# Performance work log

Hardware: AMD Instinct MI355X
Metric: run time of the kernel (lower is better)

Reference implementation:

```python
import jax, jax.numpy as jnp
import numpy as np
from jax import lax


def setup_inputs() -> dict:
    key = jax.random.key(0)
    ks = jax.random.split(key, 8)
    b, l, d_model = 2, 1024, 768
    expand, d_state, d_conv = 2, 16, 4
    d_inner = d_model * expand            # 1536
    dt_rank = -(-d_model // 16)           # ceil(768/16) = 48
    x = jax.random.normal(ks[0], (b, l, d_model), jnp.float32)
    W_in = jax.random.normal(ks[1], (d_model, 2 * d_inner), jnp.float32) * 0.02
    conv_w = jax.random.normal(ks[2], (d_inner, 1, d_conv), jnp.float32) * 0.1
    conv_b = jnp.zeros((d_inner,), jnp.float32)
    W_x = jax.random.normal(ks[3], (d_inner, dt_rank + 2 * d_state), jnp.float32) * 0.02
    W_dt = jax.random.normal(ks[4], (dt_rank, d_inner), jnp.float32) * 0.02
    b_dt = jax.random.normal(ks[5], (d_inner,), jnp.float32) * 0.02
    # A_log = log(1..d_state) broadcast over d_inner, as in the module init
    A_log = jnp.broadcast_to(jnp.log(jnp.arange(1, d_state + 1, dtype=jnp.float32)), (d_inner, d_state)).copy()
    D = jnp.ones((d_inner,), jnp.float32)
    W_out = jax.random.normal(ks[6], (d_inner, d_model), jnp.float32) * 0.02
    return {"x": x, "W_in": W_in, "conv_w": conv_w, "conv_b": conv_b, "W_x": W_x,
            "W_dt": W_dt, "b_dt": b_dt, "A_log": A_log, "D": D, "W_out": W_out}


def _silu(v):
    return v * jax.nn.sigmoid(v)


def reference(x, W_in, conv_w, conv_b, W_x, W_dt, b_dt, A_log, D, W_out):
    b, l, d_model = x.shape
    d_inner, _, d_conv = conv_w.shape
    dt_rank = W_dt.shape[0]
    n = A_log.shape[1]

    # in_proj and split into x / res paths
    x_and_res = x @ W_in                              # (b, l, 2*d_inner)
    xi, res = jnp.split(x_and_res, 2, axis=-1)

    # depthwise causal conv1d (torch pads d_conv-1 both sides then slices [:l])
    xc = jnp.transpose(xi, (0, 2, 1))                 # (b, d_inner, l)
    xc = lax.conv_general_dilated(
        xc, conv_w, window_strides=(1,), padding=[(d_conv - 1, 0)],
        dimension_numbers=("NCH", "OIH", "NCH"), feature_group_count=d_inner)
    xc = xc + conv_b[None, :, None]
    u = _silu(jnp.transpose(xc, (0, 2, 1)))           # (b, l, d_inner)

    # SSM parameters (input-dependent)
    A = -jnp.exp(A_log.astype(jnp.float32))           # (d_inner, n)
    x_dbl = u @ W_x                                   # (b, l, dt_rank + 2n)
    delta = x_dbl[..., :dt_rank]
    B = x_dbl[..., dt_rank:dt_rank + n]               # (b, l, n)
    C = x_dbl[..., dt_rank + n:]                      # (b, l, n)
    delta = jax.nn.softplus(delta @ W_dt + b_dt)      # (b, l, d_inner)

    # discretize
    deltaA = jnp.exp(delta[..., None] * A)            # (b, l, d_inner, n)
    deltaB_u = delta[..., None] * B[:, :, None, :] * u[..., None]  # (b, l, d_inner, n)

    # parallel associative scan over l: h_t = deltaA_t * h_{t-1} + deltaB_u_t
    def combine(c1, c2):
        a1, b1 = c1
        a2, b2 = c2
        return (a1 * a2, a2 * b1 + b2)

    _, hs = lax.associative_scan(combine, (deltaA, deltaB_u), axis=1)  # (b, l, d_inner, n)

    y = jnp.einsum("bldn,bln->bld", hs, C) + u * D    # (b, l, d_inner)
    y = y * _silu(res)
    out = y @ W_out                                   # (b, l, d_model)
    return out
```

## Files before the change

kernel.cpp:

```cpp
#include <hip/hip_runtime.h>
#include <math.h>

#define DI 1536
#define DM 768
#define NSTATE 16
#define DTRANK 48
#define LSEQ 1024
#define NBATCH 2
#define MROWS (NBATCH*LSEQ)
#define NXR 3072
#define NCHUNK 128
#define CLEN 8
#define SCB 128
#define DMP 16

typedef __attribute__((ext_vector_type(4))) float f32x4;
typedef __attribute__((ext_vector_type(8))) short s16x8;
typedef __attribute__((ext_vector_type(4))) unsigned int u32x4;

__device__ __forceinline__ unsigned short f2bf(float f) {
  unsigned int x = __builtin_bit_cast(unsigned int, f);
  return (unsigned short)((x + 0x7fffu + ((x >> 16) & 1u)) >> 16);
}

__device__ __forceinline__ void gload_lds16(const void* g, void* l) {
  __builtin_amdgcn_global_load_lds(
      (const __attribute__((address_space(1))) void*)g,
      (__attribute__((address_space(3))) void*)l, 16, 0, 0);
}

__global__ __launch_bounds__(256) void prep_kernel(
    const float* __restrict__ x, const float* __restrict__ W_in,
    const float* __restrict__ W_out, const float* __restrict__ W_x,
    const float* __restrict__ A_log,
    unsigned short* __restrict__ x_bf, unsigned short* __restrict__ WinT,
    unsigned short* __restrict__ WoutT, unsigned short* __restrict__ WxT,
    float* __restrict__ negA)
{
  __shared__ float t[32][33];
  const int bid = blockIdx.x;
  const int tid = threadIdx.x;
  if (bid < 768) {
    long i = ((long)bid * 256 + tid) * 8;
    f32x4 v0 = *(const f32x4*)&x[i];
    f32x4 v1 = *(const f32x4*)&x[i + 4];
    unsigned short o[8];
    #pragma unroll
    for (int j = 0; j < 4; ++j) { o[j] = f2bf(v0[j]); o[4 + j] = f2bf(v1[j]); }
    *(u32x4*)&x_bf[i] = *(u32x4*)o;
    return;
  }
  int tx = tid & 31, ty = tid >> 5;
  if (bid >= 4368) {
    int rtile = (bid - 4368) * 32;
    #pragma unroll
    for (int i = 0; i < 4; ++i) {
      int r = ty + i * 8;
      if (tx < 16) t[r][tx] = A_log[(long)(rtile + r) * NSTATE + tx];
    }
    __syncthreads();
    #pragma unroll
    for (int i = 0; i < 2; ++i) {
      int cc = ty + i * 8;
      negA[(long)cc * DI + rtile + tx] = -__expf(t[tx][cc]);
    }
    return;
  }
  const float* in; unsigned short* out; int R, C, bx, by; bool guard = false;
  if (bid < 3072)      { int q = bid - 768;  in = W_in;  out = WinT;  R = DM; C = NXR; bx = q % 96; by = q / 96; }
  else if (bid < 4224) { int q = bid - 3072; in = W_out; out = WoutT; R = DI; C = DM;  bx = q % 24; by = q / 24; }
  else                 { int q = bid - 4224; in = W_x;   out = WxT;   R = DI; C = 80;  bx = q % 3;  by = q / 3; guard = true; }
  int ctile = bx * 32, rtile = by * 32;
  #pragma unroll
  for (int i = 0; i < 4; ++i) {
    int r = ty + i * 8;
    if (!guard || (rtile + r < R && ctile + tx < C))
      t[r][tx] = in[(long)(rtile + r) * C + ctile + tx];
  }
  __syncthreads();
  #pragma unroll
  for (int i = 0; i < 4; ++i) {
    int cc = ty + i * 8;
    if (!guard || (ctile + cc < C && rtile + tx < R))
      out[(long)(ctile + cc) * R + rtile + tx] = f2bf(t[tx][cc]);
  }
}

template<int FM, int FN>
__global__ __launch_bounds__(256) void gemm_bf16(
    const unsigned short* __restrict__ A,
    const unsigned short* __restrict__ BT,
    float* __restrict__ C, int M, int N, int K)
{
  constexpr int BM = 32 * FM, BN = 32 * FN;
  constexpr int TM = BM / 16, TN = BN / 16;
  __shared__ unsigned short Ap[BM * 32];
  __shared__ unsigned short Bp[BN * 32];
  const int tid = threadIdx.x;
  const int lane = tid & 63, wave = tid >> 6;
  const int wr = wave >> 1, wc = wave & 1;
  const int lg = lane >> 4, lr = lane & 15;
  const int m0 = blockIdx.y * BM, n0 = blockIdx.x * BN;
  f32x4 acc[FM][FN] = {};
  for (int k0 = 0; k0 < K; k0 += 32) {
    #pragma unroll
    for (int p = 0; p < TM / 4; ++p) {
      int tile = wave + p * 4;
      gload_lds16(&A[(long)(m0 + tile * 16 + lr) * K + k0 + lg * 8], &Ap[tile * 512]);
    }
    #pragma unroll
    for (int p = 0; p < TN / 4; ++p) {
      int tile = wave + p * 4;
      gload_lds16(&BT[(long)(n0 + tile * 16 + lr) * K + k0 + lg * 8], &Bp[tile * 512]);
    }
    __syncthreads();
    s16x8 af[FM], bfr[FN];
    #pragma unroll
    for (int m = 0; m < FM; ++m)
      af[m] = *(s16x8*)&Ap[(((wr * FM + m) * 4 + lg) * 16 + lr) * 8];
    #pragma unroll
    for (int n = 0; n < FN; ++n)
      bfr[n] = *(s16x8*)&Bp[(((wc * FN + n) * 4 + lg) * 16 + lr) * 8];
    #pragma unroll
    for (int m = 0; m < FM; ++m)
      #pragma unroll
      for (int n = 0; n < FN; ++n)
        acc[m][n] = __builtin_amdgcn_mfma_f32_16x16x32_bf16(af[m], bfr[n], acc[m][n], 0, 0, 0);
    __syncthreads();
  }
  #pragma unroll
  for (int m = 0; m < FM; ++m)
    #pragma unroll
    for (int n = 0; n < FN; ++n)
      #pragma unroll
      for (int r = 0; r < 4; ++r) {
        int row = m0 + wr * 16 * FM + m * 16 + lg * 4 + r;
        int col = n0 + wc * 16 * FN + n * 16 + lr;
        C[(long)row * N + col] = acc[m][n][r];
      }
}

__global__ __launch_bounds__(256) void conv_silu_kernel(
    const float* __restrict__ xr,
    const float* __restrict__ conv_w,
    const float* __restrict__ conv_b,
    float* __restrict__ u,
    unsigned short* __restrict__ u_bf)
{
  int idx = blockIdx.x * 256 + threadIdx.x;
  if (idx >= MROWS * DI) return;
  int c = idx % DI;
  int bm = idx / DI;
  int t = bm % LSEQ;
  int b = bm / LSEQ;
  float w0 = conv_w[c * 4 + 0], w1 = conv_w[c * 4 + 1];
  float w2 = conv_w[c * 4 + 2], w3 = conv_w[c * 4 + 3];
  const float* xc = xr + (long)b * LSEQ * NXR + c;
  float acc = conv_b[c];
  if (t >= 3) acc = fmaf(xc[(long)(t - 3) * NXR], w0, acc);
  if (t >= 2) acc = fmaf(xc[(long)(t - 2) * NXR], w1, acc);
  if (t >= 1) acc = fmaf(xc[(long)(t - 1) * NXR], w2, acc);
  acc = fmaf(xc[(long)t * NXR], w3, acc);
  float s = acc / (1.f + __expf(-acc));
  u[idx] = s;
  u_bf[idx] = f2bf(s);
}

__global__ __launch_bounds__(256) void xdbl_mfma(
    const unsigned short* __restrict__ u_bf,
    const unsigned short* __restrict__ WxT,
    float* __restrict__ xdbl)
{
  const int tid = threadIdx.x;
  const int lane = tid & 63, wave = tid >> 6;
  const int lg = lane >> 4, lr = lane & 15;
  const int m0 = blockIdx.x * 16;
  f32x4 acc[5] = {};
  const int kbase = wave * (DI / 4);
  #pragma unroll
  for (int kk = 0; kk < DI / 4; kk += 32) {
    int k0 = kbase + kk;
    s16x8 af = *(const s16x8*)&u_bf[(long)(m0 + lr) * DI + k0 + lg * 8];
    #pragma unroll
    for (int n = 0; n < 5; ++n) {
      s16x8 bfr = *(const s16x8*)&WxT[(long)(n * 16 + lr) * DI + k0 + lg * 8];
      acc[n] = __builtin_amdgcn_mfma_f32_16x16x32_bf16(af, bfr, acc[n], 0, 0, 0);
    }
  }
  __shared__ float red[4][16][80];
  #pragma unroll
  for (int n = 0; n < 5; ++n)
    #pragma unroll
    for (int r = 0; r < 4; ++r)
      red[wave][lg * 4 + r][n * 16 + lr] = acc[n][r];
  __syncthreads();
  for (int i = tid; i < 16 * 80; i += 256) {
    int row = i / 80, col = i % 80;
    float s = red[0][row][col] + red[1][row][col] + red[2][row][col] + red[3][row][col];
    xdbl[(long)(m0 + row) * 80 + col] = s;
  }
}

__global__ __launch_bounds__(256) void delta_kernel(
    const float* __restrict__ xdbl,
    const float* __restrict__ W_dt,
    const float* __restrict__ b_dt,
    float* __restrict__ delta)
{
  __shared__ float sx[DMP][DTRANK];
  const int tid = threadIdx.x;
  const int c = blockIdx.x * 256 + tid;
  const int m0 = blockIdx.y * DMP;
  for (int i = tid; i < DMP * DTRANK; i += 256) {
    int mm = i / DTRANK, r = i % DTRANK;
    sx[mm][r] = xdbl[(long)(m0 + mm) * 80 + r];
  }
  __syncthreads();
  float bias = b_dt[c];
  float acc[DMP];
  #pragma unroll
  for (int mm = 0; mm < DMP; ++mm) acc[mm] = bias;
  for (int r = 0; r < DTRANK; ++r) {
    float wv = W_dt[(long)r * DI + c];
    #pragma unroll
    for (int mm = 0; mm < DMP; ++mm)
      acc[mm] = fmaf(sx[mm][r], wv, acc[mm]);
  }
  #pragma unroll
  for (int mm = 0; mm < DMP; ++mm) {
    float v = acc[mm];
    float sp = (v > 20.f) ? v : log1pf(__expf(v));
    delta[(long)(m0 + mm) * DI + c] = sp;
  }
}

__global__ __launch_bounds__(SCB) void scan_ph1(
    const float* __restrict__ delta,
    const float* __restrict__ xdbl,
    const float* __restrict__ u,
    const float* __restrict__ negA,
    float* __restrict__ Aprod,
    float* __restrict__ Hend)
{
  const int b = blockIdx.z, chunk = blockIdx.y;
  const int tid = threadIdx.x;
  const int d = blockIdx.x * SCB + tid;
  const long mbase = (long)b * LSEQ + chunk * CLEN;
  __shared__ float sB[CLEN][NSTATE];
  for (int i = tid; i < CLEN * NSTATE; i += SCB) {
    int t = i >> 4, j = i & 15;
    sB[t][j] = xdbl[(mbase + t) * 80 + DTRANK + j];
  }
  __syncthreads();
  float a[NSTATE];
  #pragma unroll
  for (int n = 0; n < NSTATE; ++n)
    a[n] = negA[(long)n * DI + d];
  float h[NSTATE] = {};
  float Ap[NSTATE];
  #pragma unroll
  for (int n = 0; n < NSTATE; ++n) Ap[n] = 1.f;
  #pragma unroll
  for (int t = 0; t < CLEN; ++t) {
    long m = mbase + t;
    float dt = delta[m * DI + d];
    float uu = u[m * DI + d];
    float dtu = dt * uu;
    #pragma unroll
    for (int n = 0; n < NSTATE; ++n) {
      float dA = __expf(dt * a[n]);
      Ap[n] *= dA;
      h[n] = fmaf(dA, h[n], dtu * sB[t][n]);
    }
  }
  const long o = ((long)(b * NCHUNK + chunk) * NSTATE) * DI + d;
  #pragma unroll
  for (int n = 0; n < NSTATE; ++n) {
    Aprod[o + (long)n * DI] = Ap[n];
    Hend[o + (long)n * DI] = h[n];
  }
}

__global__ __launch_bounds__(256) void scan_ph2(
    const float* __restrict__ Aprod,
    float* __restrict__ Hend)
{
  int idx = blockIdx.x * 256 + threadIdx.x;
  int b = idx / (DI * NSTATE);
  int r = idx % (DI * NSTATE);
  long o = (long)b * NCHUNK * DI * NSTATE + r;
  const long stride = (long)DI * NSTATE;
  float h = 0.f;
  for (int c = 0; c < NCHUNK; ++c) {
    float Ap = Aprod[o + c * stride];
    float He = Hend[o + c * stride];
    Hend[o + c * stride] = h;
    h = fmaf(Ap, h, He);
  }
}

__global__ __launch_bounds__(SCB) void scan_ph3(
    const float* __restrict__ delta,
    const float* __restrict__ xdbl,
    const float* __restrict__ u,
    const float* __restrict__ xr,
    const float* __restrict__ negA,
    const float* __restrict__ Dp,
    const float* __restrict__ Hstart,
    unsigned short* __restrict__ yg)
{
  const int b = blockIdx.z, chunk = blockIdx.y;
  const int tid = threadIdx.x;
  const int d = blockIdx.x * SCB + tid;
  const long mbase = (long)b * LSEQ + chunk * CLEN;
  __shared__ float sB[CLEN][NSTATE], sC[CLEN][NSTATE];
  for (int i = tid; i < CLEN * NSTATE; i += SCB) {
    int t = i >> 4, j = i & 15;
    long mo = (mbase + t) * 80 + DTRANK + j;
    sB[t][j] = xdbl[mo];
    sC[t][j] = xdbl[mo + NSTATE];
  }
  __syncthreads();
  float a[NSTATE];
  #pragma unroll
  for (int n = 0; n < NSTATE; ++n)
    a[n] = negA[(long)n * DI + d];
  const float Dv = Dp[d];
  const long o = ((long)(b * NCHUNK + chunk) * NSTATE) * DI + d;
  float h[NSTATE];
  #pragma unroll
  for (int n = 0; n < NSTATE; ++n)
    h[n] = Hstart[o + (long)n * DI];
  #pragma unroll
  for (int t = 0; t < CLEN; ++t) {
    long m = mbase + t;
    float dt = delta[m * DI + d];
    float uu = u[m * DI + d];
    float rr = xr[m * NXR + DI + d];
    float dtu = dt * uu;
    float p0 = 0.f, p1 = 0.f, p2 = 0.f, p3 = 0.f;
    #pragma unroll
    for (int q = 0; q < 4; ++q) {
      float dA0 = __expf(dt * a[q*4+0]);
      float dA1 = __expf(dt * a[q*4+1]);
      float dA2 = __expf(dt * a[q*4+2]);
      float dA3 = __expf(dt * a[q*4+3]);
      h[q*4+0] = fmaf(dA0, h[q*4+0], dtu * sB[t][q*4+0]);
      h[q*4+1] = fmaf(dA1, h[q*4+1], dtu * sB[t][q*4+1]);
      h[q*4+2] = fmaf(dA2, h[q*4+2], dtu * sB[t][q*4+2]);
      h[q*4+3] = fmaf(dA3, h[q*4+3], dtu * sB[t][q*4+3]);
    }
    #pragma unroll
    for (int n = 0; n < NSTATE; n += 4) {
      p0 = fmaf(h[n+0], sC[t][n+0], p0);
      p1 = fmaf(h[n+1], sC[t][n+1], p1);
      p2 = fmaf(h[n+2], sC[t][n+2], p2);
      p3 = fmaf(h[n+3], sC[t][n+3], p3);
    }
    float yv = (p0 + p1) + (p2 + p3) + uu * Dv;
    float gate = rr / (1.f + __expf(-rr));
    yg[m * DI + d] = f2bf(yv * gate);
  }
}

extern "C" void kernel_launch(void* const* d_in, const int* in_sizes, int n_in,
                              void* d_out, int out_size, void* d_ws, size_t ws_size,
                              hipStream_t stream)
{
  const float* x      = (const float*)d_in[0];
  const float* W_in   = (const float*)d_in[1];
  const float* conv_w = (const float*)d_in[2];
  const float* conv_b = (const float*)d_in[3];
  const float* W_x    = (const float*)d_in[4];
  const float* W_dt   = (const float*)d_in[5];
  const float* b_dt   = (const float*)d_in[6];
  const float* A_log  = (const float*)d_in[7];
  const float* Dp     = (const float*)d_in[8];
  const float* W_out  = (const float*)d_in[9];
  float* out = (float*)d_out;

  char* p = (char*)d_ws;
  float* xr     = (float*)(p + 0);
  float* u      = (float*)(p + 25165824);
  unsigned short* u_bf = (unsigned short*)(p + 37748736);
  float* xdbl   = (float*)(p + 44040192);
  float* delta  = (float*)(p + 44695552);
  float* Aprod  = (float*)(p + 57278464);
  float* Hend   = (float*)(p + 82444288);
  unsigned short* yg    = (unsigned short*)(p + 107610112);
  unsigned short* x_bf  = (unsigned short*)(p + 113901568);
  unsigned short* WinT  = (unsigned short*)(p + 117047296);
  unsigned short* WoutT = (unsigned short*)(p + 121765888);
  unsigned short* WxT   = (unsigned short*)(p + 124125184);
  float* negA   = (float*)(p + 124370944);

  prep_kernel<<<4416, 256, 0, stream>>>(x, W_in, W_out, W_x, A_log,
                                        x_bf, WinT, WoutT, WxT, negA);
  gemm_bf16<4, 4><<<dim3(NXR / 128, MROWS / 128), 256, 0, stream>>>(
      x_bf, WinT, xr, MROWS, NXR, DM);
  conv_silu_kernel<<<(MROWS * DI + 255) / 256, 256, 0, stream>>>(xr, conv_w, conv_b, u, u_bf);
  xdbl_mfma<<<MROWS / 16, 256, 0, stream>>>(u_bf, WxT, xdbl);
  delta_kernel<<<dim3(DI / 256, MROWS / DMP), 256, 0, stream>>>(xdbl, W_dt, b_dt, delta);
  scan_ph1<<<dim3(DI / SCB, NCHUNK, NBATCH), SCB, 0, stream>>>(
      delta, xdbl, u, negA, Aprod, Hend);
  scan_ph2<<<(NBATCH * DI * NSTATE) / 256, 256, 0, stream>>>(Aprod, Hend);
  scan_ph3<<<dim3(DI / SCB, NCHUNK, NBATCH), SCB, 0, stream>>>(
      delta, xdbl, u, xr, negA, Dp, Hend, yg);
  gemm_bf16<2, 2><<<dim3(DM / 64, MROWS / 64), 256, 0, stream>>>(
      yg, WoutT, out, MROWS, DM, DI);
}
```

Before: 160.1 us.

## Fuse delta projection into scan phases and shrink intermediate buffers to bf16

Removes the separate delta kernel: each scan phase now recomputes the dt projection and softplus for its chunk from xdbl in shared memory. The in-proj GEMM splits its output so the residual half is stored as bf16, and the fp32 u buffer is dropped in favour of reading u as bf16. The in-proj GEMM tile shape changes from 4x4 to 2x4 fragments. This cuts global memory traffic for the delta, u and residual intermediates, but doubles the dt computation and lowers the precision of u and res in the scan.

```diff
diff --git a/kernel.cpp b/kernel.cpp
--- a/kernel.cpp
+++ b/kernel.cpp
@@ -12,7 +12,6 @@
 #define NCHUNK 128
 #define CLEN 8
 #define SCB 128
-#define DMP 16
 
 typedef __attribute__((ext_vector_type(4))) float f32x4;
 typedef __attribute__((ext_vector_type(8))) short s16x8;
@@ -21,6 +20,10 @@
 __device__ __forceinline__ unsigned short f2bf(float f) {
   unsigned int x = __builtin_bit_cast(unsigned int, f);
   return (unsigned short)((x + 0x7fffu + ((x >> 16) & 1u)) >> 16);
+}
+__device__ __forceinline__ float bf2f(unsigned short b) {
+  unsigned int u = ((unsigned int)b) << 16;
+  return __builtin_bit_cast(float, u);
 }
 
 __device__ __forceinline__ void gload_lds16(const void* g, void* l) {
@@ -86,11 +89,13 @@
   }
 }
 
-template<int FM, int FN>
+template<int FM, int FN, bool SPLIT>
 __global__ __launch_bounds__(256) void gemm_bf16(
     const unsigned short* __restrict__ A,
     const unsigned short* __restrict__ BT,
-    float* __restrict__ C, int M, int N, int K)
+    float* __restrict__ C,
+    unsigned short* __restrict__ res_bf,
+    int M, int N, int K)
 {
   constexpr int BM = 32 * FM, BN = 32 * FN;
   constexpr int TM = BM / 16, TN = BN / 16;
@@ -136,33 +141,34 @@
       for (int r = 0; r < 4; ++r) {
         int row = m0 + wr * 16 * FM + m * 16 + lg * 4 + r;
         int col = n0 + wc * 16 * FN + n * 16 + lr;
-        C[(long)row * N + col] = acc[m][n][r];
+        if (SPLIT) {
+          if (n0 < DI) C[(long)row * DI + col] = acc[m][n][r];
+          else res_bf[(long)row * DI + col - DI] = f2bf(acc[m][n][r]);
+        } else {
+          C[(long)row * N + col] = acc[m][n][r];
+        }
       }
 }
 
 __global__ __launch_bounds__(256) void conv_silu_kernel(
-    const float* __restrict__ xr,
+    const float* __restrict__ xi,
     const float* __restrict__ conv_w,
     const float* __restrict__ conv_b,
-    float* __restrict__ u,
     unsigned short* __restrict__ u_bf)
 {
   int idx = blockIdx.x * 256 + threadIdx.x;
   if (idx >= MROWS * DI) return;
   int c = idx % DI;
-  int bm = idx / DI;
-  int t = bm % LSEQ;
-  int b = bm / LSEQ;
+  int m = idx / DI;
+  int t = m % LSEQ;
   float w0 = conv_w[c * 4 + 0], w1 = conv_w[c * 4 + 1];
   float w2 = conv_w[c * 4 + 2], w3 = conv_w[c * 4 + 3];
-  const float* xc = xr + (long)b * LSEQ * NXR + c;
   float acc = conv_b[c];
-  if (t >= 3) acc = fmaf(xc[(long)(t - 3) * NXR], w0, acc);
-  if (t >= 2) acc = fmaf(xc[(long)(t - 2) * NXR], w1, acc);
-  if (t >= 1) acc = fmaf(xc[(long)(t - 1) * NXR], w2, acc);
-  acc = fmaf(xc[(long)t * NXR], w3, acc);
+  if (t >= 3) acc = fmaf(xi[(long)(m - 3) * DI + c], w0, acc);
+  if (t >= 2) acc = fmaf(xi[(long)(m - 2) * DI + c], w1, acc);
+  if (t >= 1) acc = fmaf(xi[(long)(m - 1) * DI + c], w2, acc);
+  acc = fmaf(xi[(long)m * DI + c], w3, acc);
   float s = acc / (1.f + __expf(-acc));
-  u[idx] = s;
   u_bf[idx] = f2bf(s);
 }
 
@@ -201,44 +207,32 @@
   }
 }
 
-__global__ __launch_bounds__(256) void delta_kernel(
+__device__ __forceinline__ void chunk_dt(
+    const float* __restrict__ sX, const float* __restrict__ W_dt,
+    float bias, int d, float* dtv)
+{
+  float acc[CLEN];
+  #pragma unroll
+  for (int t = 0; t < CLEN; ++t) acc[t] = bias;
+  for (int r = 0; r < DTRANK; ++r) {
+    float wv = W_dt[(long)r * DI + d];
+    #pragma unroll
+    for (int t = 0; t < CLEN; ++t)
+      acc[t] = fmaf(sX[t * 80 + r], wv, acc[t]);
+  }
+  #pragma unroll
+  for (int t = 0; t < CLEN; ++t) {
+    float v = acc[t];
+    dtv[t] = (v > 20.f) ? v : log1pf(__expf(v));
+  }
+}
+
+__global__ __launch_bounds__(SCB) void scan_ph1(
     const float* __restrict__ xdbl,
+    const unsigned short* __restrict__ u_bf,
+    const float* __restrict__ negA,
     const float* __restrict__ W_dt,
     const float* __restrict__ b_dt,
-    float* __restrict__ delta)
-{
-  __shared__ float sx[DMP][DTRANK];
-  const int tid = threadIdx.x;
-  const int c = blockIdx.x * 256 + tid;
-  const int m0 = blockIdx.y * DMP;
-  for (int i = tid; i < DMP * DTRANK; i += 256) {
-    int mm = i / DTRANK, r = i % DTRANK;
-    sx[mm][r] = xdbl[(long)(m0 + mm) * 80 + r];
-  }
-  __syncthreads();
-  float bias = b_dt[c];
-  float acc[DMP];
-  #pragma unroll
-  for (int mm = 0; mm < DMP; ++mm) acc[mm] = bias;
-  for (int r = 0; r < DTRANK; ++r) {
-    float wv = W_dt[(long)r * DI + c];
-    #pragma unroll
-    for (int mm = 0; mm < DMP; ++mm)
-      acc[mm] = fmaf(sx[mm][r], wv, acc[mm]);
-  }
-  #pragma unroll
-  for (int mm = 0; mm < DMP; ++mm) {
-    float v = acc[mm];
-    float sp = (v > 20.f) ? v : log1pf(__expf(v));
-    delta[(long)(m0 + mm) * DI + c] = sp;
-  }
-}
-
-__global__ __launch_bounds__(SCB) void scan_ph1(
-    const float* __restrict__ delta,
-    const float* __restrict__ xdbl,
-    const float* __restrict__ u,
-    const float* __restrict__ negA,
     float* __restrict__ Aprod,
     float* __restrict__ Hend)
 {
@@ -246,12 +240,12 @@
   const int tid = threadIdx.x;
   const int d = blockIdx.x * SCB + tid;
   const long mbase = (long)b * LSEQ + chunk * CLEN;
-  __shared__ float sB[CLEN][NSTATE];
-  for (int i = tid; i < CLEN * NSTATE; i += SCB) {
-    int t = i >> 4, j = i & 15;
-    sB[t][j] = xdbl[(mbase + t) * 80 + DTRANK + j];
-  }
+  __shared__ float sX[CLEN * 80];
+  for (int i = tid; i < CLEN * 80; i += SCB)
+    sX[i] = xdbl[mbase * 80 + i];
   __syncthreads();
+  float dtv[CLEN];
+  chunk_dt(sX, W_dt, b_dt[d], d, dtv);
   float a[NSTATE];
   #pragma unroll
   for (int n = 0; n < NSTATE; ++n)
@@ -262,15 +256,14 @@
   for (int n = 0; n < NSTATE; ++n) Ap[n] = 1.f;
   #pragma unroll
   for (int t = 0; t < CLEN; ++t) {
-    long m = mbase + t;
-    float dt = delta[m * DI + d];
-    float uu = u[m * DI + d];
+    float dt = dtv[t];
+    float uu = bf2f(u_bf[(mbase + t) * DI + d]);
     float dtu = dt * uu;
     #pragma unroll
     for (int n = 0; n < NSTATE; ++n) {
       float dA = __expf(dt * a[n]);
       Ap[n] *= dA;
-      h[n] = fmaf(dA, h[n], dtu * sB[t][n]);
+      h[n] = fmaf(dA, h[n], dtu * sX[t * 80 + DTRANK + n]);
     }
   }
   const long o = ((long)(b * NCHUNK + chunk) * NSTATE) * DI + d;
@@ -300,11 +293,12 @@
 }
 
 __global__ __launch_bounds__(SCB) void scan_ph3(
-    const float* __restrict__ delta,
     const float* __restrict__ xdbl,
-    const float* __restrict__ u,
-    const float* __restrict__ xr,
+    const unsigned short* __restrict__ u_bf,
+    const unsigned short* __restrict__ res_bf,
     const float* __restrict__ negA,
+    const float* __restrict__ W_dt,
+    const float* __restrict__ b_dt,
     const float* __restrict__ Dp,
     const float* __restrict__ Hstart,
     unsigned short* __restrict__ yg)
@@ -313,14 +307,12 @@
   const int tid = threadIdx.x;
   const int d = blockIdx.x * SCB + tid;
   const long mbase = (long)b * LSEQ + chunk * CLEN;
-  __shared__ float sB[CLEN][NSTATE], sC[CLEN][NSTATE];
-  for (int i = tid; i < CLEN * NSTATE; i += SCB) {
-    int t = i >> 4, j = i & 15;
-    long mo = (mbase + t) * 80 + DTRANK + j;
-    sB[t][j] = xdbl[mo];
-    sC[t][j] = xdbl[mo + NSTATE];
-  }
+  __shared__ float sX[CLEN * 80];
+  for (int i = tid; i < CLEN * 80; i += SCB)
+    sX[i] = xdbl[mbase * 80 + i];
   __syncthreads();
+  float dtv[CLEN];
+  chunk_dt(sX, W_dt, b_dt[d], d, dtv);
   float a[NSTATE];
   #pragma unroll
   for (int n = 0; n < NSTATE; ++n)
@@ -334,9 +326,9 @@
   #pragma unroll
   for (int t = 0; t < CLEN; ++t) {
     long m = mbase + t;
-    float dt = delta[m * DI + d];
-    float uu = u[m * DI + d];
-    float rr = xr[m * NXR + DI + d];
+    float dt = dtv[t];
+    float uu = bf2f(u_bf[m * DI + d]);
+    float rr = bf2f(res_bf[m * DI + d]);
     float dtu = dt * uu;
     float p0 = 0.f, p1 = 0.f, p2 = 0.f, p3 = 0.f;
     #pragma unroll
@@ -345,17 +337,17 @@
       float dA1 = __expf(dt * a[q*4+1]);
       float dA2 = __expf(dt * a[q*4+2]);
       float dA3 = __expf(dt * a[q*4+3]);
-      h[q*4+0] = fmaf(dA0, h[q*4+0], dtu * sB[t][q*4+0]);
-      h[q*4+1] = fmaf(dA1, h[q*4+1], dtu * sB[t][q*4+1]);
-      h[q*4+2] = fmaf(dA2, h[q*4+2], dtu * sB[t][q*4+2]);
-      h[q*4+3] = fmaf(dA3, h[q*4+3], dtu * sB[t][q*4+3]);
+      h[q*4+0] = fmaf(dA0, h[q*4+0], dtu * sX[t*80 + DTRANK + q*4+0]);
+      h[q*4+1] = fmaf(dA1, h[q*4+1], dtu * sX[t*80 + DTRANK + q*4+1]);
+      h[q*4+2] = fmaf(dA2, h[q*4+2], dtu * sX[t*80 + DTRANK + q*4+2]);
+      h[q*4+3] = fmaf(dA3, h[q*4+3], dtu * sX[t*80 + DTRANK + q*4+3]);
     }
     #pragma unroll
     for (int n = 0; n < NSTATE; n += 4) {
-      p0 = fmaf(h[n+0], sC[t][n+0], p0);
-      p1 = fmaf(h[n+1], sC[t][n+1], p1);
-      p2 = fmaf(h[n+2], sC[t][n+2], p2);
-      p3 = fmaf(h[n+3], sC[t][n+3], p3);
+      p0 = fmaf(h[n+0], sX[t*80 + 64 + n+0], p0);
+      p1 = fmaf(h[n+1], sX[t*80 + 64 + n+1], p1);
+      p2 = fmaf(h[n+2], sX[t*80 + 64 + n+2], p2);
+      p3 = fmaf(h[n+3], sX[t*80 + 64 + n+3], p3);
     }
     float yv = (p0 + p1) + (p2 + p3) + uu * Dv;
     float gate = rr / (1.f + __expf(-rr));
@@ -380,32 +372,31 @@
   float* out = (float*)d_out;
 
   char* p = (char*)d_ws;
-  float* xr     = (float*)(p + 0);
-  float* u      = (float*)(p + 25165824);
-  unsigned short* u_bf = (unsigned short*)(p + 37748736);
-  float* xdbl   = (float*)(p + 44040192);
-  float* delta  = (float*)(p + 44695552);
-  float* Aprod  = (float*)(p + 57278464);
-  float* Hend   = (float*)(p + 82444288);
-  unsigned short* yg    = (unsigned short*)(p + 107610112);
-  unsigned short* x_bf  = (unsigned short*)(p + 113901568);
-  unsigned short* WinT  = (unsigned short*)(p + 117047296);
-  unsigned short* WoutT = (unsigned short*)(p + 121765888);
-  unsigned short* WxT   = (unsigned short*)(p + 124125184);
-  float* negA   = (float*)(p + 124370944);
+  float* xi     = (float*)(p + 0);
+  unsigned short* res_bf = (unsigned short*)(p + 12582912);
+  unsigned short* u_bf   = (unsigned short*)(p + 18874368);
+  float* xdbl   = (float*)(p + 25165824);
+  float* Aprod  = (float*)(p + 25821184);
+  float* Hend   = (float*)(p + 50987008);
+  unsigned short* yg    = (unsigned short*)(p + 76152832);
+  unsigned short* x_bf  = (unsigned short*)(p + 82444288);
+  unsigned short* WinT  = (unsigned short*)(p + 85590016);
+  unsigned short* WoutT = (unsigned short*)(p + 90308608);
+  unsigned short* WxT   = (unsigned short*)(p + 92667904);
+  float* negA   = (float*)(p + 92913664);
 
   prep_kernel<<<4416, 256, 0, stream>>>(x, W_in, W_out, W_x, A_log,
                                         x_bf, WinT, WoutT, WxT, negA);
-  gemm_bf16<4, 4><<<dim3(NXR / 128, MROWS / 128), 256, 0, stream>>>(
-      x_bf, WinT, xr, MROWS, NXR, DM);
-  conv_silu_kernel<<<(MROWS * DI + 255) / 256, 256, 0, stream>>>(xr, conv_w, conv_b, u, u_bf);
+  gemm_bf16<2, 4, true><<<dim3(NXR / 128, MROWS / 64), 256, 0, stream>>>(
+      x_bf, WinT, xi, res_bf, MROWS, NXR, DM);
+  conv_silu_kernel<<<(MROWS * DI + 255) / 256, 256, 0, stream>>>(
+      xi, conv_w, conv_b, u_bf);
   xdbl_mfma<<<MROWS / 16, 256, 0, stream>>>(u_bf, WxT, xdbl);
-  delta_kernel<<<dim3(DI / 256, MROWS / DMP), 256, 0, stream>>>(xdbl, W_dt, b_dt, delta);
   scan_ph1<<<dim3(DI / SCB, NCHUNK, NBATCH), SCB, 0, stream>>>(
-      delta, xdbl, u, negA, Aprod, Hend);
+      xdbl, u_bf, negA, W_dt, b_dt, Aprod, Hend);
   scan_ph2<<<(NBATCH * DI * NSTATE) / 256, 256, 0, stream>>>(Aprod, Hend);
   scan_ph3<<<dim3(DI / SCB, NCHUNK, NBATCH), SCB, 0, stream>>>(
-      delta, xdbl, u, xr, negA, Dp, Hend, yg);
-  gemm_bf16<2, 2><<<dim3(DM / 64, MROWS / 64), 256, 0, stream>>>(
-      yg, WoutT, out, MROWS, DM, DI);
-}
+      xdbl, u_bf, res_bf, negA, W_dt, b_dt, Dp, Hend, yg);
+  gemm_bf16<2, 2, false><<<dim3(DM / 64, MROWS / 64), 256, 0, stream>>>(
+      yg, WoutT, out, nullptr, MROWS, DM, DI);
+}
```

Result: slower. 227.1 us (+41.8%).

## Split in_proj output into fp32 xi and bf16 res, drop fp32 u buffer

Applied to the files above, without the earlier changes.

The in_proj GEMM epilogue now writes the xi half as fp32 in a compact DI-stride layout and the res half directly as bf16. The conv kernel no longer stores an fp32 copy of u, and the scan kernels read u and res as bf16. The in_proj GEMM tile also changes from 128x128 to 64x128 blocks. This cuts global memory traffic across several kernels, at the cost of using bf16-rounded u and res inside the scan.

```diff
diff --git a/kernel.cpp b/kernel.cpp
--- a/kernel.cpp
+++ b/kernel.cpp
@@ -22,6 +22,10 @@
   unsigned int x = __builtin_bit_cast(unsigned int, f);
   return (unsigned short)((x + 0x7fffu + ((x >> 16) & 1u)) >> 16);
 }
+__device__ __forceinline__ float bf2f(unsigned short b) {
+  unsigned int u = ((unsigned int)b) << 16;
+  return __builtin_bit_cast(float, u);
+}
 
 __device__ __forceinline__ void gload_lds16(const void* g, void* l) {
   __builtin_amdgcn_global_load_lds(
@@ -86,11 +90,13 @@
   }
 }
 
-template<int FM, int FN>
+template<int FM, int FN, bool SPLIT>
 __global__ __launch_bounds__(256) void gemm_bf16(
     const unsigned short* __restrict__ A,
     const unsigned short* __restrict__ BT,
-    float* __restrict__ C, int M, int N, int K)
+    float* __restrict__ C,
+    unsigned short* __restrict__ res_bf,
+    int M, int N, int K)
 {
   constexpr int BM = 32 * FM, BN = 32 * FN;
   constexpr int TM = BM / 16, TN = BN / 16;
@@ -136,33 +142,34 @@
       for (int r = 0; r < 4; ++r) {
         int row = m0 + wr * 16 * FM + m * 16 + lg * 4 + r;
         int col = n0 + wc * 16 * FN + n * 16 + lr;
-        C[(long)row * N + col] = acc[m][n][r];
+        if (SPLIT) {
+          if (n0 < DI) C[(long)row * DI + col] = acc[m][n][r];
+          else res_bf[(long)row * DI + col - DI] = f2bf(acc[m][n][r]);
+        } else {
+          C[(long)row * N + col] = acc[m][n][r];
+        }
       }
 }
 
 __global__ __launch_bounds__(256) void conv_silu_kernel(
-    const float* __restrict__ xr,
+    const float* __restrict__ xi,
     const float* __restrict__ conv_w,
     const float* __restrict__ conv_b,
-    float* __restrict__ u,
     unsigned short* __restrict__ u_bf)
 {
   int idx = blockIdx.x * 256 + threadIdx.x;
   if (idx >= MROWS * DI) return;
   int c = idx % DI;
-  int bm = idx / DI;
-  int t = bm % LSEQ;
-  int b = bm / LSEQ;
+  int m = idx / DI;
+  int t = m % LSEQ;
   float w0 = conv_w[c * 4 + 0], w1 = conv_w[c * 4 + 1];
   float w2 = conv_w[c * 4 + 2], w3 = conv_w[c * 4 + 3];
-  const float* xc = xr + (long)b * LSEQ * NXR + c;
   float acc = conv_b[c];
-  if (t >= 3) acc = fmaf(xc[(long)(t - 3) * NXR], w0, acc);
-  if (t >= 2) acc = fmaf(xc[(long)(t - 2) * NXR], w1, acc);
-  if (t >= 1) acc = fmaf(xc[(long)(t - 1) * NXR], w2, acc);
-  acc = fmaf(xc[(long)t * NXR], w3, acc);
+  if (t >= 3) acc = fmaf(xi[(long)(m - 3) * DI + c], w0, acc);
+  if (t >= 2) acc = fmaf(xi[(long)(m - 2) * DI + c], w1, acc);
+  if (t >= 1) acc = fmaf(xi[(long)(m - 1) * DI + c], w2, acc);
+  acc = fmaf(xi[(long)m * DI + c], w3, acc);
   float s = acc / (1.f + __expf(-acc));
-  u[idx] = s;
   u_bf[idx] = f2bf(s);
 }
 
@@ -237,7 +244,7 @@
 __global__ __launch_bounds__(SCB) void scan_ph1(
     const float* __restrict__ delta,
     const float* __restrict__ xdbl,
-    const float* __restrict__ u,
+    const unsigned short* __restrict__ u_bf,
     const float* __restrict__ negA,
     float* __restrict__ Aprod,
     float* __restrict__ Hend)
@@ -264,7 +271,7 @@
   for (int t = 0; t < CLEN; ++t) {
     long m = mbase + t;
     float dt = delta[m * DI + d];
-    float uu = u[m * DI + d];
+    float uu = bf2f(u_bf[m * DI + d]);
     float dtu = dt * uu;
     #pragma unroll
     for (int n = 0; n < NSTATE; ++n) {
@@ -302,8 +309,8 @@
 __global__ __launch_bounds__(SCB) void scan_ph3(
     const float* __restrict__ delta,
     const float* __restrict__ xdbl,
-    const float* __restrict__ u,
-    const float* __restrict__ xr,
+    const unsigned short* __restrict__ u_bf,
+    const unsigned short* __restrict__ res_bf,
     const float* __restrict__ negA,
     const float* __restrict__ Dp,
     const float* __restrict__ Hstart,
@@ -335,8 +342,8 @@
   for (int t = 0; t < CLEN; ++t) {
     long m = mbase + t;
     float dt = delta[m * DI + d];
-    float uu = u[m * DI + d];
-    float rr = xr[m * NXR + DI + d];
+    float uu = bf2f(u_bf[m * DI + d]);
+    float rr = bf2f(res_bf[m * DI + d]);
     float dtu = dt * uu;
     float p0 = 0.f, p1 = 0.f, p2 = 0.f, p3 = 0.f;
     #pragma unroll
@@ -380,32 +387,33 @@
   float* out = (float*)d_out;
 
   char* p = (char*)d_ws;
-  float* xr     = (float*)(p + 0);
-  float* u      = (float*)(p + 25165824);
-  unsigned short* u_bf = (unsigned short*)(p + 37748736);
-  float* xdbl   = (float*)(p + 44040192);
-  float* delta  = (float*)(p + 44695552);
-  float* Aprod  = (float*)(p + 57278464);
-  float* Hend   = (float*)(p + 82444288);
-  unsigned short* yg    = (unsigned short*)(p + 107610112);
-  unsigned short* x_bf  = (unsigned short*)(p + 113901568);
-  unsigned short* WinT  = (unsigned short*)(p + 117047296);
-  unsigned short* WoutT = (unsigned short*)(p + 121765888);
-  unsigned short* WxT   = (unsigned short*)(p + 124125184);
-  float* negA   = (float*)(p + 124370944);
+  float* xi     = (float*)(p + 0);
+  unsigned short* res_bf = (unsigned short*)(p + 12582912);
+  unsigned short* u_bf   = (unsigned short*)(p + 18874368);
+  float* xdbl   = (float*)(p + 25165824);
+  float* delta  = (float*)(p + 25821184);
+  float* Aprod  = (float*)(p + 38404096);
+  float* Hend   = (float*)(p + 63569920);
+  unsigned short* yg    = (unsigned short*)(p + 88735744);
+  unsigned short* x_bf  = (unsigned short*)(p + 95027200);
+  unsigned short* WinT  = (unsigned short*)(p + 98172928);
+  unsigned short* WoutT = (unsigned short*)(p + 102891520);
+  unsigned short* WxT   = (unsigned short*)(p + 105250816);
+  float* negA   = (float*)(p + 105496576);
 
   prep_kernel<<<4416, 256, 0, stream>>>(x, W_in, W_out, W_x, A_log,
                                         x_bf, WinT, WoutT, WxT, negA);
-  gemm_bf16<4, 4><<<dim3(NXR / 128, MROWS / 128), 256, 0, stream>>>(
-      x_bf, WinT, xr, MROWS, NXR, DM);
-  conv_silu_kernel<<<(MROWS * DI + 255) / 256, 256, 0, stream>>>(xr, conv_w, conv_b, u, u_bf);
+  gemm_bf16<2, 4, true><<<dim3(NXR / 128, MROWS / 64), 256, 0, stream>>>(
+      x_bf, WinT, xi, res_bf, MROWS, NXR, DM);
+  conv_silu_kernel<<<(MROWS * DI + 255) / 256, 256, 0, stream>>>(
+      xi, conv_w, conv_b, u_bf);
   xdbl_mfma<<<MROWS / 16, 256, 0, stream>>>(u_bf, WxT, xdbl);
   delta_kernel<<<dim3(DI / 256, MROWS / DMP), 256, 0, stream>>>(xdbl, W_dt, b_dt, delta);
   scan_ph1<<<dim3(DI / SCB, NCHUNK, NBATCH), SCB, 0, stream>>>(
-      delta, xdbl, u, negA, Aprod, Hend);
+      delta, xdbl, u_bf, negA, Aprod, Hend);
   scan_ph2<<<(NBATCH * DI * NSTATE) / 256, 256, 0, stream>>>(Aprod, Hend);
   scan_ph3<<<dim3(DI / SCB, NCHUNK, NBATCH), SCB, 0, stream>>>(
-      delta, xdbl, u, xr, negA, Dp, Hend, yg);
-  gemm_bf16<2, 2><<<dim3(DM / 64, MROWS / 64), 256, 0, stream>>>(
-      yg, WoutT, out, MROWS, DM, DI);
-}
+      delta, xdbl, u_bf, res_bf, negA, Dp, Hend, yg);
+  gemm_bf16<2, 2, false><<<dim3(DM / 64, MROWS / 64), 256, 0, stream>>>(
+      yg, WoutT, out, nullptr, MROWS, DM, DI);
+}
```

New measurement: 160.7 us (median of 2 runs). No clear change (+0.3%).
